# Performance work log

Measured on AMD Instinct MI355X. Metric: run time of the kernel, lower is better.

The kernel has to match this reference:

```python
import jax, jax.numpy as jnp
import numpy as np

MU = 1.0  # opts.loss_type[1]


def setup_inputs() -> dict:
    key = jax.random.key(0)
    k1, k2 = jax.random.split(key)
    B, D, N = 8, 3, 4096
    srcs = jax.random.normal(k1, (B, D, N), dtype=jnp.float32)
    tgts = jax.random.normal(k2, (B, D, N), dtype=jnp.float32)
    return {"srcs": srcs, "tgts": tgts}


def reference(srcs, tgts):
    # [B, D, N] -> [B, N, D]
    s = jnp.transpose(srcs, (0, 2, 1))
    t = jnp.transpose(tgts, (0, 2, 1))
    # squared euclidean pairwise distances: ||s_i - t_j||^2, [B, N, M]
    s_sq = jnp.sum(s * s, axis=-1)          # [B, N]
    t_sq = jnp.sum(t * t, axis=-1)          # [B, M]
    cross = jnp.einsum('bnd,bmd->bnm', s, t)  # [B, N, M]
    P = s_sq[:, :, None] + t_sq[:, None, :] - 2.0 * cross
    # bidirectional chamfer mins
    d_tgt = jnp.min(P, axis=1)  # min over src points, [B, M]
    d_src = jnp.min(P, axis=2)  # min over tgt points, [B, N]
    distances = jnp.stack([d_tgt, d_src], axis=-1)  # [B, N, 2]
    # Geman-McClure robust penalty
    losses = (MU * distances / (distances + MU)).sum(axis=2).mean(axis=1).mean()
    return losses
```

## Files before the change

kernel.cpp:

```cpp
#include <hip/hip_runtime.h>


#define NPTS 4096
#define NB 8

__global__ __launch_bounds__(1024, 8)
void chamfer_gm_kernel(const float* __restrict__ srcs,
                       const float* __restrict__ tgts,
                       float* __restrict__ out) {
    __shared__ float4 sDB[NPTS];

    const int blk  = blockIdx.x;
    const int pair = blk >> 5;
    const int sub  = blk & 31;
    const int dir  = pair >> 3;
    const int b    = pair & 7;

    const float* qg = (dir == 0 ? srcs : tgts) + b * 3 * NPTS;
    const float* dg = (dir == 0 ? tgts : srcs) + b * 3 * NPTS;

    const int tid = threadIdx.x;

#pragma unroll
    for (int r = 0; r < 4; r++) {
        const int j = tid + r * 1024;
        const float x = dg[j];
        const float y = dg[NPTS + j];
        const float z = dg[2 * NPTS + j];
        sDB[j] = make_float4(-2.0f * x, -2.0f * y, -2.0f * z,
                             fmaf(z, z, fmaf(y, y, x * x)));
    }

    const int wave  = tid >> 6;
    const int lane  = tid & 63;
    const int qbase = sub * 128 + wave * 8;

    float qx[8], qy[8], qz[8], dmin[8];
#pragma unroll
    for (int q = 0; q < 8; q++) {
        qx[q] = qg[qbase + q];
        qy[q] = qg[NPTS + qbase + q];
        qz[q] = qg[2 * NPTS + qbase + q];
        dmin[q] = 3.0e38f;
    }
    __syncthreads();

#pragma unroll 2
    for (int it = 0; it < NPTS / 64; it++) {
        const float4 t = sDB[it * 64 + lane];
#pragma unroll
        for (int q = 0; q < 8; q++) {
            const float v = fmaf(qx[q], t.x,
                           fmaf(qy[q], t.y,
                           fmaf(qz[q], t.z, t.w)));
            dmin[q] = fminf(dmin[q], v);
        }
    }

    float acc = 0.0f;
#pragma unroll
    for (int q = 0; q < 8; q++) {
        float m = dmin[q];
#pragma unroll
        for (int off = 32; off > 0; off >>= 1)
            m = fminf(m, __shfl_xor(m, off, 64));
        const float qs = fmaf(qz[q], qz[q], fmaf(qy[q], qy[q], qx[q] * qx[q]));
        float d = fmaxf(m + qs, 0.0f);
        acc += d / (d + 1.0f);
    }

    __syncthreads();
    float* sPart = (float*)sDB;
    if (lane == 0) sPart[wave] = acc;
    __syncthreads();
    if (tid == 0) {
        float s = 0.0f;
#pragma unroll
        for (int w = 0; w < 16; w++) s += sPart[w];
        atomicAdd(out, s * (1.0f / (NB * NPTS)));
    }
}

extern "C" void kernel_launch(void* const* d_in, const int* in_sizes, int n_in,
                              void* d_out, int out_size, void* d_ws, size_t ws_size,
                              hipStream_t stream) {
    const float* srcs = (const float*)d_in[0];
    const float* tgts = (const float*)d_in[1];
    float* out = (float*)d_out;
    chamfer_gm_kernel<<<dim3(512), dim3(1024), 0, stream>>>(srcs, tgts, out);
}
```

Baseline: 81.34 us.

## Precompute transformed point database in workspace and stream it from global memory

A separate pre-pass writes the transformed (-2x,-2y,-2z,|p|^2) float4 database for every batch and direction into workspace once. The main kernel then reads it from global/L2 with software-prefetched registers instead of having each block rebuild it in LDS. Blocks shrink to 256 threads and each wave handles 16 queries, which raises reuse of every loaded point. Partial sums go into per-group padded cells and a final single-thread kernel reduces them, at the cost of two extra launches and more register pressure.

```diff
diff --git a/kernel.cpp b/kernel.cpp
--- a/kernel.cpp
+++ b/kernel.cpp
@@ -3,63 +3,78 @@
 
 #define NPTS 4096
 #define NB 8
+#define QW 16
 
-__global__ __launch_bounds__(1024, 8)
+__global__ __launch_bounds__(256)
+void transform_kernel(const float* __restrict__ srcs,
+                      const float* __restrict__ tgts,
+                      float4* __restrict__ ws4) {
+    const int gid = blockIdx.x * 256 + threadIdx.x;
+    const int dir = gid >> 15;
+    const int rem = gid & 32767;
+    const int b   = rem >> 12;
+    const int j   = rem & 4095;
+    const float* dg = (dir == 0 ? tgts : srcs) + b * 3 * NPTS;
+    const float x = dg[j], y = dg[NPTS + j], z = dg[2 * NPTS + j];
+    ws4[gid] = make_float4(-2.0f * x, -2.0f * y, -2.0f * z,
+                           fmaf(z, z, fmaf(y, y, x * x)));
+    if (gid < 256) ((float*)(ws4 + 2 * NB * NPTS))[gid] = 0.0f;
+}
+
+#define COMP(T)                                                         \
+    _Pragma("unroll")                                                   \
+    for (int q = 0; q < QW; q++) {                                      \
+        dmin[q] = fminf(dmin[q],                                        \
+            fmaf(qx[q], (T).x, fmaf(qy[q], (T).y,                       \
+            fmaf(qz[q], (T).z, (T).w))));                               \
+    }
+
+__global__ __launch_bounds__(256, 4)
 void chamfer_gm_kernel(const float* __restrict__ srcs,
                        const float* __restrict__ tgts,
-                       float* __restrict__ out) {
-    __shared__ float4 sDB[NPTS];
+                       const float4* __restrict__ dbws,
+                       float* __restrict__ cells) {
+    __shared__ float sPart[4];
 
-    const int blk  = blockIdx.x;
-    const int pair = blk >> 5;
-    const int sub  = blk & 31;
-    const int dir  = pair >> 3;
-    const int b    = pair & 7;
+    const int blk   = blockIdx.x;
+    const int group = blk & 15;
+    const int chunk = blk >> 4;
+    const int dir   = group >> 3;
+    const int b     = group & 7;
 
-    const float* qg = (dir == 0 ? srcs : tgts) + b * 3 * NPTS;
-    const float* dg = (dir == 0 ? tgts : srcs) + b * 3 * NPTS;
+    const float* qg  = (dir == 0 ? srcs : tgts) + b * 3 * NPTS;
+    const float4* db = dbws + group * NPTS;
 
-    const int tid = threadIdx.x;
+    const int wave  = threadIdx.x >> 6;
+    const int lane  = threadIdx.x & 63;
+    const int qbase = chunk * 64 + wave * QW;
 
+    float qx[QW], qy[QW], qz[QW], dmin[QW];
 #pragma unroll
-    for (int r = 0; r < 4; r++) {
-        const int j = tid + r * 1024;
-        const float x = dg[j];
-        const float y = dg[NPTS + j];
-        const float z = dg[2 * NPTS + j];
-        sDB[j] = make_float4(-2.0f * x, -2.0f * y, -2.0f * z,
-                             fmaf(z, z, fmaf(y, y, x * x)));
-    }
-
-    const int wave  = tid >> 6;
-    const int lane  = tid & 63;
-    const int qbase = sub * 128 + wave * 8;
-
-    float qx[8], qy[8], qz[8], dmin[8];
-#pragma unroll
-    for (int q = 0; q < 8; q++) {
+    for (int q = 0; q < QW; q++) {
         qx[q] = qg[qbase + q];
         qy[q] = qg[NPTS + qbase + q];
         qz[q] = qg[2 * NPTS + qbase + q];
         dmin[q] = 3.0e38f;
     }
-    __syncthreads();
 
-#pragma unroll 2
-    for (int it = 0; it < NPTS / 64; it++) {
-        const float4 t = sDB[it * 64 + lane];
-#pragma unroll
-        for (int q = 0; q < 8; q++) {
-            const float v = fmaf(qx[q], t.x,
-                           fmaf(qy[q], t.y,
-                           fmaf(qz[q], t.z, t.w)));
-            dmin[q] = fminf(dmin[q], v);
-        }
+    float4 t0 = db[lane];
+    float4 t1 = db[64 + lane];
+    float4 t2 = db[128 + lane];
+    float4 t3 = db[192 + lane];
+    for (int it = 0; it < 60; it += 4) {
+        const float4 n0 = db[(it + 4) * 64 + lane];
+        const float4 n1 = db[(it + 5) * 64 + lane];
+        const float4 n2 = db[(it + 6) * 64 + lane];
+        const float4 n3 = db[(it + 7) * 64 + lane];
+        COMP(t0); COMP(t1); COMP(t2); COMP(t3);
+        t0 = n0; t1 = n1; t2 = n2; t3 = n3;
     }
+    COMP(t0); COMP(t1); COMP(t2); COMP(t3);
 
     float acc = 0.0f;
 #pragma unroll
-    for (int q = 0; q < 8; q++) {
+    for (int q = 0; q < QW; q++) {
         float m = dmin[q];
 #pragma unroll
         for (int off = 32; off > 0; off >>= 1)
@@ -68,16 +83,21 @@
         float d = fmaxf(m + qs, 0.0f);
         acc += d / (d + 1.0f);
     }
-
-    __syncthreads();
-    float* sPart = (float*)sDB;
     if (lane == 0) sPart[wave] = acc;
     __syncthreads();
-    if (tid == 0) {
+    if (threadIdx.x == 0) {
+        atomicAdd(&cells[group * 16],
+                  sPart[0] + sPart[1] + sPart[2] + sPart[3]);
+    }
+}
+
+__global__ void finish_kernel(const float* __restrict__ cells,
+                              float* __restrict__ out) {
+    if (threadIdx.x == 0) {
         float s = 0.0f;
 #pragma unroll
-        for (int w = 0; w < 16; w++) s += sPart[w];
-        atomicAdd(out, s * (1.0f / (NB * NPTS)));
+        for (int i = 0; i < 16; i++) s += cells[i * 16];
+        out[0] = s * (1.0f / (NB * NPTS));
     }
 }
 
@@ -86,6 +106,11 @@
                               hipStream_t stream) {
     const float* srcs = (const float*)d_in[0];
     const float* tgts = (const float*)d_in[1];
-    float* out = (float*)d_out;
-    chamfer_gm_kernel<<<dim3(512), dim3(1024), 0, stream>>>(srcs, tgts, out);
+    float* out  = (float*)d_out;
+    float4* ws4 = (float4*)d_ws;
+    float* cells = (float*)(ws4 + 2 * NB * NPTS);
+
+    transform_kernel<<<dim3(256), dim3(256), 0, stream>>>(srcs, tgts, ws4);
+    chamfer_gm_kernel<<<dim3(1024), dim3(256), 0, stream>>>(srcs, tgts, ws4, cells);
+    finish_kernel<<<dim3(1), dim3(64), 0, stream>>>(cells, out);
 }
```

After: 83.50 us. +2.7%, slower.
